# Kernel tuning notes

Hardware: AMD Instinct MI355X
Metric: run time of the kernel (lower is better)

## Reference

```python
import jax, jax.numpy as jnp
import numpy as np
import math

B, N, D_MODEL, D_QK, D_V = 8, 2048, 512, 64, 64
NEG_INF = float('-inf')

def setup_inputs() -> dict:
    key = jax.random.key(0)
    k1, k2, k3, k4, k5 = jax.random.split(key, 5)
    mask = jax.random.randint(k1, (B, N, N), 0, 2).astype(bool)
    x_key_value = jax.random.normal(k2, (B, N, D_MODEL), dtype=jnp.float32)
    wk = jax.random.normal(k3, (D_MODEL, D_QK), dtype=jnp.float32) * 0.02
    wq = jax.random.normal(k4, (D_MODEL, D_QK), dtype=jnp.float32) * 0.02
    wv = jax.random.normal(k5, (D_MODEL, D_V), dtype=jnp.float32) * 0.02
    return {"mask": mask, "x_key_value": x_key_value, "wk": wk, "wq": wq, "wv": wv}

def reference(mask, x_key_value, wk, wq, wv):
    # self-attention: x_query defaults to x_key_value
    div = math.sqrt(wk.shape[1])
    k = x_key_value @ wk          # [n, j, d_qk]
    q = x_key_value @ wq          # [n, i, d_qk]
    v = x_key_value @ wv          # [n, j, d_v]
    mat = jnp.einsum('nik,njk->nij', q, k) / div
    mat = jnp.where(mask, mat, NEG_INF)
    portion = jax.nn.softmax(mat, axis=2)
    return jnp.einsum('nij,njk->nik', portion, v)
```

## Files before the change

kernel.cpp:

```cpp
#include <hip/hip_runtime.h>
#include <hip/hip_bf16.h>

typedef __attribute__((ext_vector_type(8))) short bf16x8;
typedef __attribute__((ext_vector_type(4))) float f32x4;
typedef __hip_bfloat16 bf16;

#define BATCH 8
#define SEQ   2048
#define DMODEL 512
#define DHEAD 64
#define ROWS (BATCH * SEQ)
#define LOG2E 1.44269504f

static __device__ inline short f2bf(float f) {
    union { __hip_bfloat16 h; short s; } u;
    u.h = __float2bfloat16(f);
    return u.s;
}

__global__ __launch_bounds__(256) void transpose_w_kernel(
    const float* __restrict__ wq, const float* __restrict__ wk,
    const float* __restrict__ wv, bf16* __restrict__ wt)
{
    const int s  = blockIdx.x / 8;
    const int kt = blockIdx.x % 8;
    const float* w = (s == 0) ? wq : ((s == 1) ? wk : wv);

    __shared__ float Ts[64][68];

    const int tid = threadIdx.x;
    int nr = tid >> 4;
    int n4 = (tid & 15) * 4;
#pragma unroll
    for (int p = 0; p < 4; ++p) {
        int k = 16 * p + nr;
        float4 v = *(const float4*)(w + (size_t)(kt * 64 + k) * DHEAD + n4);
        Ts[k][n4] = v.x; Ts[k][n4 + 1] = v.y; Ts[k][n4 + 2] = v.z; Ts[k][n4 + 3] = v.w;
    }
    __syncthreads();
#pragma unroll
    for (int p = 0; p < 2; ++p) {
        int cc = tid + p * 256;
        int n = cc >> 3;
        int kk = (cc & 7) * 8;
        bf16x8 o;
#pragma unroll
        for (int e = 0; e < 8; ++e) o[e] = f2bf(Ts[kk + e][n]);
        *(bf16x8*)(wt + (size_t)(s * 64 + n) * DMODEL + kt * 64 + kk) = o;
    }
}

__global__ __launch_bounds__(512) void proj_kernel(
    const float* __restrict__ x, const bf16* __restrict__ wt,
    bf16* __restrict__ Q, bf16* __restrict__ K, bf16* __restrict__ Vt)
{
    const int r0 = blockIdx.x * 32;
    const int tid = threadIdx.x;
    const int lane = tid & 63;
    const int wid = tid >> 6;
    const int strip = wid & 1;
    const int cq = wid >> 1;
    const int l15 = lane & 15;
    const int quad = lane >> 4;

    f32x4 acc[3] = {};

    const float* xp = x + (size_t)(r0 + 16 * strip + l15) * DMODEL;

    for (int k0 = 0; k0 < DMODEL; k0 += 64) {
        float4 xa = *(const float4*)(xp + k0 + quad * 8);
        float4 xb = *(const float4*)(xp + k0 + quad * 8 + 4);
        float4 xc = *(const float4*)(xp + k0 + 32 + quad * 8);
        float4 xd = *(const float4*)(xp + k0 + 32 + quad * 8 + 4);
        bf16x8 a0, a1;
        a0[0] = f2bf(xa.x); a0[1] = f2bf(xa.y); a0[2] = f2bf(xa.z); a0[3] = f2bf(xa.w);
        a0[4] = f2bf(xb.x); a0[5] = f2bf(xb.y); a0[6] = f2bf(xb.z); a0[7] = f2bf(xb.w);
        a1[0] = f2bf(xc.x); a1[1] = f2bf(xc.y); a1[2] = f2bf(xc.z); a1[3] = f2bf(xc.w);
        a1[4] = f2bf(xd.x); a1[5] = f2bf(xd.y); a1[6] = f2bf(xd.z); a1[7] = f2bf(xd.w);
#pragma unroll
        for (int g = 0; g < 3; ++g) {
            int n = 16 * (3 * cq + g) + l15;
            const bf16* wp = wt + (size_t)n * DMODEL + k0 + quad * 8;
            bf16x8 b0 = *(const bf16x8*)(wp);
            bf16x8 b1 = *(const bf16x8*)(wp + 32);
            acc[g] = __builtin_amdgcn_mfma_f32_16x16x32_bf16(a0, b0, acc[g], 0, 0, 0);
            acc[g] = __builtin_amdgcn_mfma_f32_16x16x32_bf16(a1, b1, acc[g], 0, 0, 0);
        }
    }

#pragma unroll
    for (int g = 0; g < 3; ++g) {
        int ng = 16 * (3 * cq + g) + l15;
        int sel = ng >> 6;
        int col = ng & 63;
#pragma unroll
        for (int r = 0; r < 4; ++r) {
            int row = r0 + 16 * strip + quad * 4 + r;
            union { __hip_bfloat16 h; bf16 b; } u;
            u.h = __float2bfloat16(acc[g][r]);
            if (sel == 0)      Q[(size_t)row * DHEAD + col] = u.b;
            else if (sel == 1) K[(size_t)row * DHEAD + col] = u.b;
            else {
                int bb = row >> 11, j = row & (SEQ - 1);
                Vt[((size_t)bb * DHEAD + col) * SEQ + j] = u.b;
            }
        }
    }
}

__global__ __launch_bounds__(256) void flash_kernel(
    const bf16* __restrict__ Q, const bf16* __restrict__ K,
    const bf16* __restrict__ Vt, const int* __restrict__ mask,
    float* __restrict__ out)
{
    const int b = blockIdx.y;
    const int q0 = blockIdx.x * 16;
    const int tid = threadIdx.x;
    const int lane = tid & 63;
    const int wid = tid >> 6;
    const int l15 = lane & 15;
    const int quad = lane >> 4;

    __shared__ __align__(16) bf16 Ps[4][16][72];
    __shared__ float Om[4][16][64];
    __shared__ float Mw[4][16];
    __shared__ float Lw[4][16];

    const bf16* qp = Q + ((size_t)(b * SEQ + q0 + l15)) * DHEAD + quad * 8;
    bf16x8 aQ0 = *(const bf16x8*)(qp);
    bf16x8 aQ1 = *(const bf16x8*)(qp + 32);

    f32x4 oacc[4] = {};
    float m_i[4], l_i[4];
#pragma unroll
    for (int r = 0; r < 4; ++r) { m_i[r] = -1e30f; l_i[r] = 0.f; }

    const int* mp = mask + ((size_t)(b * SEQ + q0 + quad * 4)) * SEQ;
    const int jbase = wid * (SEQ / 4);

    for (int jt = 0; jt < SEQ / 4; jt += 64) {
        const int j0 = jbase + jt;

        f32x4 sacc[4] = {};
#pragma unroll
        for (int c = 0; c < 4; ++c) {
            const bf16* kp = K + ((size_t)(b * SEQ + j0 + 16 * c + l15)) * DHEAD + quad * 8;
            bf16x8 b0 = *(const bf16x8*)(kp);
            bf16x8 b1 = *(const bf16x8*)(kp + 32);
            sacc[c] = __builtin_amdgcn_mfma_f32_16x16x32_bf16(aQ0, b0, sacc[c], 0, 0, 0);
            sacc[c] = __builtin_amdgcn_mfma_f32_16x16x32_bf16(aQ1, b1, sacc[c], 0, 0, 0);
        }

#pragma unroll
        for (int c = 0; c < 4; ++c) {
#pragma unroll
            for (int r = 0; r < 4; ++r) {
                int mv = mp[(size_t)r * SEQ + (j0 + 16 * c + l15)];
                sacc[c][r] = mv ? sacc[c][r] * 0.125f : -1e30f;
            }
        }

#pragma unroll
        for (int r = 0; r < 4; ++r) {
            float rm = fmaxf(fmaxf(sacc[0][r], sacc[1][r]), fmaxf(sacc[2][r], sacc[3][r]));
            rm = fmaxf(rm, __shfl_xor(rm, 1));
            rm = fmaxf(rm, __shfl_xor(rm, 2));
            rm = fmaxf(rm, __shfl_xor(rm, 4));
            rm = fmaxf(rm, __shfl_xor(rm, 8));
            float mn = fmaxf(m_i[r], rm);
            float alpha = exp2f((m_i[r] - mn) * LOG2E);
            m_i[r] = mn;
            float rs = 0.f;
#pragma unroll
            for (int c = 0; c < 4; ++c) {
                float pv = exp2f((sacc[c][r] - mn) * LOG2E);
                sacc[c][r] = pv;
                rs += pv;
            }
            rs += __shfl_xor(rs, 1);
            rs += __shfl_xor(rs, 2);
            rs += __shfl_xor(rs, 4);
            rs += __shfl_xor(rs, 8);
            l_i[r] = l_i[r] * alpha + rs;
#pragma unroll
            for (int c = 0; c < 4; ++c) oacc[c][r] *= alpha;
        }

#pragma unroll
        for (int c = 0; c < 4; ++c)
#pragma unroll
            for (int r = 0; r < 4; ++r) {
                union { __hip_bfloat16 h; bf16 b; } u;
                u.h = __float2bfloat16(sacc[c][r]);
                Ps[wid][quad * 4 + r][16 * c + l15] = u.b;
            }

        bf16x8 aP0 = *(const bf16x8*)(&Ps[wid][l15][quad * 8]);
        bf16x8 aP1 = *(const bf16x8*)(&Ps[wid][l15][32 + quad * 8]);
#pragma unroll
        for (int c = 0; c < 4; ++c) {
            const bf16* vp = Vt + ((size_t)b * DHEAD + 16 * c + l15) * SEQ + j0 + quad * 8;
            bf16x8 v0 = *(const bf16x8*)(vp);
            bf16x8 v1 = *(const bf16x8*)(vp + 32);
            oacc[c] = __builtin_amdgcn_mfma_f32_16x16x32_bf16(aP0, v0, oacc[c], 0, 0, 0);
            oacc[c] = __builtin_amdgcn_mfma_f32_16x16x32_bf16(aP1, v1, oacc[c], 0, 0, 0);
        }
    }

#pragma unroll
    for (int c = 0; c < 4; ++c)
#pragma unroll
        for (int r = 0; r < 4; ++r)
            Om[wid][quad * 4 + r][16 * c + l15] = oacc[c][r];
    if (l15 == 0) {
#pragma unroll
        for (int r = 0; r < 4; ++r) {
            Mw[wid][quad * 4 + r] = m_i[r];
            Lw[wid][quad * 4 + r] = l_i[r];
        }
    }
    __syncthreads();

    {
        int row = tid >> 4;
        int c0 = (tid & 15) * 4;
        float M = fmaxf(fmaxf(Mw[0][row], Mw[1][row]), fmaxf(Mw[2][row], Mw[3][row]));
        float sc0 = exp2f((Mw[0][row] - M) * LOG2E);
        float sc1 = exp2f((Mw[1][row] - M) * LOG2E);
        float sc2 = exp2f((Mw[2][row] - M) * LOG2E);
        float sc3 = exp2f((Mw[3][row] - M) * LOG2E);
        float L = Lw[0][row] * sc0 + Lw[1][row] * sc1 + Lw[2][row] * sc2 + Lw[3][row] * sc3;
        float invL = 1.0f / L;
        float4 o;
        float* op = (float*)&o;
#pragma unroll
        for (int e = 0; e < 4; ++e) {
            op[e] = (Om[0][row][c0 + e] * sc0 + Om[1][row][c0 + e] * sc1 +
                     Om[2][row][c0 + e] * sc2 + Om[3][row][c0 + e] * sc3) * invL;
        }
        *(float4*)(out + ((size_t)(b * SEQ + q0 + row)) * DHEAD + c0) = o;
    }
}

extern "C" void kernel_launch(void* const* d_in, const int* in_sizes, int n_in,
                              void* d_out, int out_size, void* d_ws, size_t ws_size,
                              hipStream_t stream)
{
    const int*   mask = (const int*)d_in[0];
    const float* x    = (const float*)d_in[1];
    const float* wk   = (const float*)d_in[2];
    const float* wq   = (const float*)d_in[3];
    const float* wv   = (const float*)d_in[4];
    float* out = (float*)d_out;

    bf16* Qb = (bf16*)d_ws;
    bf16* Kb = Qb + (size_t)ROWS * DHEAD;
    bf16* Vt = Kb + (size_t)ROWS * DHEAD;
    bf16* Wt = Vt + (size_t)BATCH * DHEAD * SEQ;

    transpose_w_kernel<<<dim3(24), 256, 0, stream>>>(wq, wk, wv, Wt);
    proj_kernel<<<dim3(ROWS / 32), 512, 0, stream>>>(x, Wt, Qb, Kb, Vt);
    flash_kernel<<<dim3(SEQ / 16, BATCH), 256, 0, stream>>>(Qb, Kb, Vt, mask, out);
}
```

Measured before the change: 300.4 us.

## Pack boolean mask into bitmasks inside projection kernel, read bits in flash kernel

Extra blocks appended to the projection kernel convert the int32 mask into 64-bit bitmasks, one bit per key position. The flash kernel then loads one 64-bit word per row per tile instead of scattered int32 mask elements. The mask still has to be read in full once, but the attention loop's mask traffic becomes much smaller and far less scattered. The cost is an added pass with a workspace write and some extra shift-and-test work per element.

```diff
diff --git a/kernel.cpp b/kernel.cpp
--- a/kernel.cpp
+++ b/kernel.cpp
@@ -11,6 +11,9 @@
 #define DHEAD 64
 #define ROWS (BATCH * SEQ)
 #define LOG2E 1.44269504f
+
+#define PROJ_BLOCKS (ROWS / 32)
+#define PACK_BLOCKS 1024
 
 static __device__ inline short f2bf(float f) {
     union { __hip_bfloat16 h; short s; } u;
@@ -50,10 +53,36 @@
     }
 }
 
-__global__ __launch_bounds__(512) void proj_kernel(
+__global__ __launch_bounds__(512) void proj_pack_kernel(
     const float* __restrict__ x, const bf16* __restrict__ wt,
-    bf16* __restrict__ Q, bf16* __restrict__ K, bf16* __restrict__ Vt)
+    const int* __restrict__ mask,
+    bf16* __restrict__ Q, bf16* __restrict__ K, bf16* __restrict__ Vt,
+    unsigned long long* __restrict__ mb)
 {
+    if (blockIdx.x >= PROJ_BLOCKS) {
+        const int t = (blockIdx.x - PROJ_BLOCKS) * 512 + threadIdx.x;
+        const int4* mp4 = (const int4*)(mask + (size_t)t * 64);
+        unsigned int lo = 0, hi = 0;
+#pragma unroll
+        for (int p = 0; p < 8; ++p) {
+            int4 v = mp4[p];
+            lo |= (unsigned)(v.x != 0) << (4 * p);
+            lo |= (unsigned)(v.y != 0) << (4 * p + 1);
+            lo |= (unsigned)(v.z != 0) << (4 * p + 2);
+            lo |= (unsigned)(v.w != 0) << (4 * p + 3);
+        }
+#pragma unroll
+        for (int p = 8; p < 16; ++p) {
+            int4 v = mp4[p];
+            hi |= (unsigned)(v.x != 0) << (4 * (p - 8));
+            hi |= (unsigned)(v.y != 0) << (4 * (p - 8) + 1);
+            hi |= (unsigned)(v.z != 0) << (4 * (p - 8) + 2);
+            hi |= (unsigned)(v.w != 0) << (4 * (p - 8) + 3);
+        }
+        mb[t] = ((unsigned long long)hi << 32) | (unsigned long long)lo;
+        return;
+    }
+
     const int r0 = blockIdx.x * 32;
     const int tid = threadIdx.x;
     const int lane = tid & 63;
@@ -110,7 +139,7 @@
 
 __global__ __launch_bounds__(256) void flash_kernel(
     const bf16* __restrict__ Q, const bf16* __restrict__ K,
-    const bf16* __restrict__ Vt, const int* __restrict__ mask,
+    const bf16* __restrict__ Vt, const unsigned long long* __restrict__ mb,
     float* __restrict__ out)
 {
     const int b = blockIdx.y;
@@ -135,11 +164,15 @@
 #pragma unroll
     for (int r = 0; r < 4; ++r) { m_i[r] = -1e30f; l_i[r] = 0.f; }
 
-    const int* mp = mask + ((size_t)(b * SEQ + q0 + quad * 4)) * SEQ;
+    const unsigned long long* mrow = mb + ((size_t)(b * SEQ + q0 + quad * 4)) * 32;
     const int jbase = wid * (SEQ / 4);
 
     for (int jt = 0; jt < SEQ / 4; jt += 64) {
         const int j0 = jbase + jt;
+
+        unsigned long long mrw[4];
+#pragma unroll
+        for (int r = 0; r < 4; ++r) mrw[r] = mrow[(size_t)r * 32 + (j0 >> 6)];
 
         f32x4 sacc[4] = {};
 #pragma unroll
@@ -152,12 +185,14 @@
         }
 
 #pragma unroll
-        for (int c = 0; c < 4; ++c) {
-#pragma unroll
-            for (int r = 0; r < 4; ++r) {
-                int mv = mp[(size_t)r * SEQ + (j0 + 16 * c + l15)];
-                sacc[c][r] = mv ? sacc[c][r] * 0.125f : -1e30f;
-            }
+        for (int r = 0; r < 4; ++r) {
+            unsigned long long mr = mrw[r] >> l15;
+            unsigned m0 = (unsigned)mr;
+            unsigned m1 = (unsigned)(mr >> 32);
+            sacc[0][r] = (m0 & 1u)         ? sacc[0][r] * 0.125f : -1e30f;
+            sacc[1][r] = ((m0 >> 16) & 1u) ? sacc[1][r] * 0.125f : -1e30f;
+            sacc[2][r] = (m1 & 1u)         ? sacc[2][r] * 0.125f : -1e30f;
+            sacc[3][r] = ((m1 >> 16) & 1u) ? sacc[3][r] * 0.125f : -1e30f;
         }
 
 #pragma unroll
@@ -257,8 +292,10 @@
     bf16* Kb = Qb + (size_t)ROWS * DHEAD;
     bf16* Vt = Kb + (size_t)ROWS * DHEAD;
     bf16* Wt = Vt + (size_t)BATCH * DHEAD * SEQ;
+    unsigned long long* Mb = (unsigned long long*)(Wt + 3 * (size_t)DHEAD * DMODEL);
 
     transpose_w_kernel<<<dim3(24), 256, 0, stream>>>(wq, wk, wv, Wt);
-    proj_kernel<<<dim3(ROWS / 32), 512, 0, stream>>>(x, Wt, Qb, Kb, Vt);
-    flash_kernel<<<dim3(SEQ / 16, BATCH), 256, 0, stream>>>(Qb, Kb, Vt, mask, out);
-}
+    proj_pack_kernel<<<dim3(PROJ_BLOCKS + PACK_BLOCKS), 512, 0, stream>>>(
+        x, Wt, mask, Qb, Kb, Vt, Mb);
+    flash_kernel<<<dim3(SEQ / 16, BATCH), 256, 0, stream>>>(Qb, Kb, Vt, Mb, out);
+}
```

Result: slower. 317.9 us (+5.8%).

## Prefetch mask with coalesced loads and pack into double-buffered LDS bitmasks

Applied to the files above, without the earlier changes.

Mask loads change from scattered per-lane int reads (16 lanes per row, strided) to fully coalesced 256-wide row reads by the whole block. Each row chunk is compressed into 64-bit ballot bitmasks stored in double-buffered shared memory, and the next tile's mask is prefetched one iteration ahead. Each warp now covers interleaved 64-column chunks instead of a contiguous quarter of the sequence. The aim is to cut mask memory traffic inefficiency, which dominates because the mask is stored as int32. The cost is a block-wide __syncthreads on every iteration and extra registers for the prefetched values.

```diff
diff --git a/kernel.cpp b/kernel.cpp
--- a/kernel.cpp
+++ b/kernel.cpp
@@ -125,6 +125,7 @@
     __shared__ float Om[4][16][64];
     __shared__ float Mw[4][16];
     __shared__ float Lw[4][16];
+    __shared__ __align__(16) unsigned int WtM[2][16][10];
 
     const bf16* qp = Q + ((size_t)(b * SEQ + q0 + l15)) * DHEAD + quad * 8;
     bf16x8 aQ0 = *(const bf16x8*)(qp);
@@ -135,11 +136,30 @@
 #pragma unroll
     for (int r = 0; r < 4; ++r) { m_i[r] = -1e30f; l_i[r] = 0.f; }
 
-    const int* mp = mask + ((size_t)(b * SEQ + q0 + quad * 4)) * SEQ;
-    const int jbase = wid * (SEQ / 4);
-
-    for (int jt = 0; jt < SEQ / 4; jt += 64) {
-        const int j0 = jbase + jt;
+    const int* mbase = mask + ((size_t)(b * SEQ + q0)) * SEQ;
+
+    {
+        int v[16];
+#pragma unroll
+        for (int i = 0; i < 16; ++i) v[i] = mbase[(size_t)i * SEQ + tid];
+#pragma unroll
+        for (int i = 0; i < 16; ++i) {
+            unsigned long long bal = __ballot(v[i] != 0);
+            if (lane == 0) *(unsigned long long*)&WtM[0][i][2 * wid] = bal;
+        }
+    }
+    __syncthreads();
+
+    for (int kk = 0; kk < 8; ++kk) {
+        const int buf = kk & 1;
+        const int j0 = 256 * kk + 64 * wid;
+
+        int v[16];
+        if (kk < 7) {
+#pragma unroll
+            for (int i = 0; i < 16; ++i)
+                v[i] = mbase[(size_t)i * SEQ + 256 * (kk + 1) + tid];
+        }
 
         f32x4 sacc[4] = {};
 #pragma unroll
@@ -152,12 +172,15 @@
         }
 
 #pragma unroll
-        for (int c = 0; c < 4; ++c) {
-#pragma unroll
-            for (int r = 0; r < 4; ++r) {
-                int mv = mp[(size_t)r * SEQ + (j0 + 16 * c + l15)];
-                sacc[c][r] = mv ? sacc[c][r] * 0.125f : -1e30f;
-            }
+        for (int r = 0; r < 4; ++r) {
+            unsigned long long mr =
+                *(const unsigned long long*)&WtM[buf][quad * 4 + r][2 * wid] >> l15;
+            unsigned m0 = (unsigned)mr;
+            unsigned m1 = (unsigned)(mr >> 32);
+            sacc[0][r] = (m0 & 1u)         ? sacc[0][r] * 0.125f : -1e30f;
+            sacc[1][r] = ((m0 >> 16) & 1u) ? sacc[1][r] * 0.125f : -1e30f;
+            sacc[2][r] = (m1 & 1u)         ? sacc[2][r] * 0.125f : -1e30f;
+            sacc[3][r] = ((m1 >> 16) & 1u) ? sacc[3][r] * 0.125f : -1e30f;
         }
 
 #pragma unroll
@@ -205,6 +228,15 @@
             oacc[c] = __builtin_amdgcn_mfma_f32_16x16x32_bf16(aP0, v0, oacc[c], 0, 0, 0);
             oacc[c] = __builtin_amdgcn_mfma_f32_16x16x32_bf16(aP1, v1, oacc[c], 0, 0, 0);
         }
+
+        if (kk < 7) {
+#pragma unroll
+            for (int i = 0; i < 16; ++i) {
+                unsigned long long bal = __ballot(v[i] != 0);
+                if (lane == 0) *(unsigned long long*)&WtM[buf ^ 1][i][2 * wid] = bal;
+            }
+        }
+        __syncthreads();
     }
 
 #pragma unroll
```

After: 289.0 us. -3.8%, faster.

## Load mask rows coalesced, redistribute via ballot, and prefetch next tile

Applied to the files above, without the earlier changes.

Each lane now loads the mask with one contiguous int per row across the 64 columns of a tile, where before every lane gathered scattered elements. The bits are turned into per-lane masks with wave ballots and shifts. The next tile's mask loads are issued early and K loads are hoisted ahead of the MFMAs with a sched barrier, so memory latency overlaps compute. The cost is more registers for the prefetched mask values and K fragments, plus 16 ballots per tile.

```diff
diff --git a/kernel.cpp b/kernel.cpp
--- a/kernel.cpp
+++ b/kernel.cpp
@@ -135,29 +135,57 @@
 #pragma unroll
     for (int r = 0; r < 4; ++r) { m_i[r] = -1e30f; l_i[r] = 0.f; }
 
-    const int* mp = mask + ((size_t)(b * SEQ + q0 + quad * 4)) * SEQ;
     const int jbase = wid * (SEQ / 4);
-
-    for (int jt = 0; jt < SEQ / 4; jt += 64) {
-        const int j0 = jbase + jt;
-
-        f32x4 sacc[4] = {};
+    const int* mrow0 = mask + ((size_t)(b * SEQ + q0)) * SEQ + jbase;
+
+    int v[16];
+#pragma unroll
+    for (int i = 0; i < 16; ++i) v[i] = mrow0[(size_t)i * SEQ + lane];
+
+    for (int kk = 0; kk < 8; ++kk) {
+        const int j0 = jbase + kk * 64;
+
+        unsigned long long bal[16];
+#pragma unroll
+        for (int i = 0; i < 16; ++i) bal[i] = __ballot(v[i] != 0);
+        unsigned long long mrw[4];
+#pragma unroll
+        for (int r = 0; r < 4; ++r) {
+            unsigned long long b01 = (quad & 1) ? bal[4 + r]  : bal[r];
+            unsigned long long b23 = (quad & 1) ? bal[12 + r] : bal[8 + r];
+            mrw[r] = ((quad & 2) ? b23 : b01) >> l15;
+        }
+
+        bf16x8 kb[8];
 #pragma unroll
         for (int c = 0; c < 4; ++c) {
             const bf16* kp = K + ((size_t)(b * SEQ + j0 + 16 * c + l15)) * DHEAD + quad * 8;
-            bf16x8 b0 = *(const bf16x8*)(kp);
-            bf16x8 b1 = *(const bf16x8*)(kp + 32);
-            sacc[c] = __builtin_amdgcn_mfma_f32_16x16x32_bf16(aQ0, b0, sacc[c], 0, 0, 0);
-            sacc[c] = __builtin_amdgcn_mfma_f32_16x16x32_bf16(aQ1, b1, sacc[c], 0, 0, 0);
-        }
-
+            kb[2 * c]     = *(const bf16x8*)(kp);
+            kb[2 * c + 1] = *(const bf16x8*)(kp + 32);
+        }
+        __builtin_amdgcn_sched_barrier(0);
+
+        if (kk < 7) {
+#pragma unroll
+            for (int i = 0; i < 16; ++i)
+                v[i] = mrow0[(size_t)i * SEQ + (kk + 1) * 64 + lane];
+        }
+
+        f32x4 sacc[4] = {};
 #pragma unroll
         for (int c = 0; c < 4; ++c) {
-#pragma unroll
-            for (int r = 0; r < 4; ++r) {
-                int mv = mp[(size_t)r * SEQ + (j0 + 16 * c + l15)];
-                sacc[c][r] = mv ? sacc[c][r] * 0.125f : -1e30f;
-            }
+            sacc[c] = __builtin_amdgcn_mfma_f32_16x16x32_bf16(aQ0, kb[2 * c],     sacc[c], 0, 0, 0);
+            sacc[c] = __builtin_amdgcn_mfma_f32_16x16x32_bf16(aQ1, kb[2 * c + 1], sacc[c], 0, 0, 0);
+        }
+
+#pragma unroll
+        for (int r = 0; r < 4; ++r) {
+            unsigned m0 = (unsigned)mrw[r];
+            unsigned m1 = (unsigned)(mrw[r] >> 32);
+            sacc[0][r] = (m0 & 1u)         ? sacc[0][r] * 0.125f : -1e30f;
+            sacc[1][r] = ((m0 >> 16) & 1u) ? sacc[1][r] * 0.125f : -1e30f;
+            sacc[2][r] = (m1 & 1u)         ? sacc[2][r] * 0.125f : -1e30f;
+            sacc[3][r] = ((m1 >> 16) & 1u) ? sacc[3][r] * 0.125f : -1e30f;
         }
 
 #pragma unroll
```

Result: slower. 359.3 us (+19.6%).
